# Kernel tuning notes

Measured on AMD Instinct MI355X. Metric: run time of the kernel, lower is better.

Reference implementation:

```python
import jax, jax.numpy as jnp
import numpy as np

B, L, D, DK, DV = 8, 2048, 1024, 1024, 1024

def setup_inputs() -> dict:
    key = jax.random.key(0)
    ks = jax.random.split(key, 8)
    # scale inputs/weights down so exp(scores) is numerically stable
    # (original softmax has no max-subtraction)
    x = jax.random.normal(ks[0], (B, L, D), dtype=jnp.float32) * 0.05
    Wq = jax.random.normal(ks[1], (D, DK), dtype=jnp.float32) * 0.05
    bq = jax.random.normal(ks[2], (DK,), dtype=jnp.float32) * 0.05
    Wk = jax.random.normal(ks[3], (D, DK), dtype=jnp.float32) * 0.05
    bk = jax.random.normal(ks[4], (DK,), dtype=jnp.float32) * 0.05
    Wv = jax.random.normal(ks[5], (D, DV), dtype=jnp.float32) * 0.05
    bv = jax.random.normal(ks[6], (DV,), dtype=jnp.float32) * 0.05
    actulength = jax.random.randint(ks[7], (B,), 1, L, dtype=jnp.int32)
    return {"x": x, "actulength": actulength, "Wq": Wq, "bq": bq,
            "Wk": Wk, "bk": bk, "Wv": Wv, "bv": bv}

def reference(x, actulength, Wq, bq, Wk, bk, Wv, bv):
    # QKV projections
    Q = x @ Wq + bq                      # [B, L, DK]
    K = x @ Wk + bk                      # [B, L, DK]
    V = x @ Wv + bv                      # [B, L, DV]
    scale = 1.0 / jnp.sqrt(jnp.float32(DK))
    scores = jnp.einsum('bld,bmd->blm', Q, K) * scale  # [B, L, L]
    # custom padding-aware softmax: subtract padding count from the sum
    s = jnp.exp(scores)
    tsum = jnp.sum(s, axis=2)            # [B, L]
    padding = (L - actulength).astype(s.dtype)[:, None]  # [B, 1]
    atten = s / (tsum - padding)[:, :, None]
    return jnp.einsum('blm,bmv->blv', atten, V)  # [B, L, DV]
```

## Files before the change

### kernel.cpp

```cpp
#include <hip/hip_runtime.h>
#include <hip/hip_bf16.h>
#include <cstdint>

#define DEV __device__ __forceinline__

typedef __attribute__((ext_vector_type(8))) __bf16 bf16x8;
typedef __attribute__((ext_vector_type(4))) float f32x4;

DEV ushort f2bf(float f){
  uint32_t u = __builtin_bit_cast(uint32_t, f);
  u += 0x7fffu + ((u >> 16) & 1u);
  return (ushort)(u >> 16);
}

DEV void gll16(const void* g, void* l){
  __builtin_amdgcn_global_load_lds((const __attribute__((address_space(1))) void*)g,
                                   (__attribute__((address_space(3))) void*)l, 16, 0, 0);
}

template<int MODE>
__global__ __launch_bounds__(512, 2) void gemm256(
    const ushort* __restrict__ A, const ushort* __restrict__ Bt,
    const float* __restrict__ bias,
    ushort* __restrict__ Cb, float* __restrict__ Cf,
    int gm, int gn, int K, int lda, int ldb, int ldc,
    size_t sA, size_t sB, size_t sC,
    float scale, float* __restrict__ partial, const float* __restrict__ denom,
    int Mrows, int nch)
{
  __shared__ __align__(16) ushort As[4][128][64];
  __shared__ __align__(16) ushort Bs[4][128][64];

  const int tid  = threadIdx.x;
  const int lane = tid & 63, wid = tid >> 6;
  const int wm = wid >> 2, wn = wid & 3;
  const int lr = lane & 15, fq = lane >> 4;
  const int lrh = lr >> 1;
  const int lo2 = ((lane & 1) << 2) | fq;

  const int nwg = gridDim.x;
  const int per = nwg >> 3;
  const int id  = blockIdx.x;
  const int swz = (id & 7) * per + (id >> 3);
  const int gmn = gm * gn;
  const int bz  = swz / gmn;
  const int rr  = swz - bz * gmn;
  const int bn  = rr / gm;
  const int bm  = rr - bn * gm;

  const ushort* Ab = A  + (size_t)bz * sA + (size_t)bm * 256 * (size_t)lda;
  const ushort* Bb = Bt + (size_t)bz * sB + (size_t)bn * 256 * (size_t)ldb;
  const int NT = K >> 5;

  auto stageA = [&](int t){
    const int s = t & 3;
    const size_t kb = (size_t)t * 64;
#pragma unroll
    for (int q = 0; q < 2; ++q){
      int c = q*512 + tid;
      int R = c >> 3, ci = c & 7;
      int u = ci ^ (R & 7);
      size_t sb = (size_t)(2*R + (u >> 2)) * (size_t)(lda*2) + kb + (size_t)((u & 3) << 4);
      gll16((const char*)Ab + sb,
            (ushort*)As + (size_t)s*8192 + (size_t)(q*512 + (wid << 6))*8);
    }
  };
  auto stageB = [&](int t){
    const int s = t & 3;
    const size_t kb = (size_t)t * 64;
#pragma unroll
    for (int q = 0; q < 2; ++q){
      int c = q*512 + tid;
      int R = c >> 3, ci = c & 7;
      int u = ci ^ (R & 7);
      size_t sb = (size_t)(2*R + (u >> 2)) * (size_t)(ldb*2) + kb + (size_t)((u & 3) << 4);
      gll16((const char*)Bb + sb,
            (ushort*)Bs + (size_t)s*8192 + (size_t)(q*512 + (wid << 6))*8);
    }
  };

  f32x4 acc[8][4];
  const f32x4 z = {0.f, 0.f, 0.f, 0.f};
#pragma unroll
  for (int m = 0; m < 8; ++m)
#pragma unroll
    for (int n = 0; n < 4; ++n) acc[m][n] = z;

  const int cio  = (lo2 ^ lrh) << 3;
  const int aoff = (wm*64 + lrh)*64 + cio;
  const int boff = (wn*32 + lrh)*64 + cio;

  stageA(0); stageB(0); stageA(1); stageB(1);
  asm volatile("s_waitcnt vmcnt(4)" ::: "memory");
  __builtin_amdgcn_s_barrier();

  for (int t = 0; t < NT; ++t){
    const int s = t & 3;
    const ushort* Asl = (const ushort*)As + (size_t)s*8192;
    const ushort* Bsl = (const ushort*)Bs + (size_t)s*8192;
    const bool pre = (t + 2 < NT);

    bf16x8 bfv[4], af0[4];
#pragma unroll
    for (int n = 0; n < 4; ++n)
      bfv[n] = *(const bf16x8*)&Bsl[boff + n*512];
#pragma unroll
    for (int m = 0; m < 4; ++m)
      af0[m] = *(const bf16x8*)&Asl[aoff + m*512];
    if (pre) stageA(t + 2);
    __builtin_amdgcn_s_barrier();
    asm volatile("s_waitcnt lgkmcnt(0)" ::: "memory");
    __builtin_amdgcn_sched_barrier(0);
    __builtin_amdgcn_s_setprio(1);
#pragma unroll
    for (int m = 0; m < 4; ++m)
#pragma unroll
      for (int n = 0; n < 4; ++n)
        acc[m][n] = __builtin_amdgcn_mfma_f32_16x16x32_bf16(af0[m], bfv[n], acc[m][n], 0, 0, 0);
    __builtin_amdgcn_s_setprio(0);
    __builtin_amdgcn_s_barrier();

    bf16x8 af1[4];
#pragma unroll
    for (int m = 0; m < 4; ++m)
      af1[m] = *(const bf16x8*)&Asl[aoff + (m + 4)*512];
    if (pre) stageB(t + 2);
    __builtin_amdgcn_s_barrier();
    asm volatile("s_waitcnt lgkmcnt(0)" ::: "memory");
    __builtin_amdgcn_sched_barrier(0);
    __builtin_amdgcn_s_setprio(1);
#pragma unroll
    for (int m = 0; m < 4; ++m)
#pragma unroll
      for (int n = 0; n < 4; ++n)
        acc[m + 4][n] = __builtin_amdgcn_mfma_f32_16x16x32_bf16(af1[m], bfv[n], acc[m + 4][n], 0, 0, 0);
    __builtin_amdgcn_s_setprio(0);

    if (t < NT - 1){
      if (t + 2 < NT) asm volatile("s_waitcnt vmcnt(4)" ::: "memory");
      else            asm volatile("s_waitcnt vmcnt(0)" ::: "memory");
      __builtin_amdgcn_s_barrier();
    }
  }

  const int rbase = bm*256 + wm*128 + fq*4;
  const int cbase = bn*256 + wn*64 + lr;

  if (MODE == 0){
    ushort* dst = Cb + (size_t)bz * sC;
#pragma unroll
    for (int m = 0; m < 8; ++m){
      int r0 = rbase + m*16;
#pragma unroll
      for (int n = 0; n < 4; ++n){
        int c = cbase + n*16;
        float bvv = bias[c];
#pragma unroll
        for (int i = 0; i < 4; ++i)
          dst[(size_t)(r0 + i)*ldc + c] = f2bf(acc[m][n][i] + bvv);
      }
    }
  } else if (MODE == 1){
    ushort* dst = Cb + (size_t)bz * sC;
#pragma unroll
    for (int m = 0; m < 8; ++m){
      int r0 = rbase + m*16;
#pragma unroll
      for (int i = 0; i < 4; ++i){
        int r = r0 + i;
        float rs = 0.f;
#pragma unroll
        for (int n = 0; n < 4; ++n){
          float v = __expf(acc[m][n][i] * scale);
          dst[(size_t)r*ldc + cbase + n*16] = f2bf(v);
          rs += v;
        }
        rs += __shfl_xor(rs, 1);
        rs += __shfl_xor(rs, 2);
        rs += __shfl_xor(rs, 4);
        rs += __shfl_xor(rs, 8);
        if (lr == 0)
          partial[((size_t)bz*Mrows + r)*nch + (bn*4 + wn)] = rs;
      }
    }
  } else {
    float* dst = Cf + (size_t)bz * sC;
#pragma unroll
    for (int m = 0; m < 8; ++m){
      int r0 = rbase + m*16;
#pragma unroll
      for (int i = 0; i < 4; ++i){
        int r = r0 + i;
        float inv = 1.0f / denom[(size_t)bz*Mrows + r];
#pragma unroll
        for (int n = 0; n < 4; ++n)
          dst[(size_t)r*ldc + cbase + n*16] = acc[m][n][i] * inv;
      }
    }
  }
}


__global__ void denom_k(const float* __restrict__ partial, const int* __restrict__ alen,
                        float* __restrict__ denom, int L, int nch){
  int i = blockIdx.x*blockDim.x + threadIdx.x;
  int b = i / L;
  const float* p = partial + (size_t)i*nch;
  float s = 0.f;
  for (int j = 0; j < nch; j++) s += p[j];
  denom[i] = s - (float)(L - alen[b]);
}

__global__ void cvt_f32_bf16(const float* __restrict__ in, ushort* __restrict__ out, long n4){
  long i = (long)blockIdx.x*blockDim.x + threadIdx.x;
  if (i >= n4) return;
  float4 f = ((const float4*)in)[i];
  ushort4 u;
  u.x = f2bf(f.x); u.y = f2bf(f.y); u.z = f2bf(f.z); u.w = f2bf(f.w);
  ((ushort4*)out)[i] = u;
}

__global__ __launch_bounds__(256) void transpose_f32_bf16(
    const float* __restrict__ in, ushort* __restrict__ out, int R, int C){
  __shared__ ushort t[32][33];
  int tx = threadIdx.x, ty = threadIdx.y;
  int c0 = blockIdx.x*32, r0 = blockIdx.y*32;
#pragma unroll
  for (int i = 0; i < 4; i++)
    t[ty + i*8][tx] = f2bf(in[(size_t)(r0 + ty + i*8)*C + c0 + tx]);
  __syncthreads();
#pragma unroll
  for (int i = 0; i < 4; i++)
    out[(size_t)(c0 + ty + i*8)*R + r0 + tx] = t[tx][ty + i*8];
}

__global__ __launch_bounds__(256) void transpose_v(
    const ushort* __restrict__ qkv, ushort* __restrict__ vt,
    int L_, int DV_, int ldq){
  __shared__ ushort tbuf[32][33];
  int bz = blockIdx.z;
  const ushort* src = qkv + (size_t)bz*L_*ldq + 2048;
  ushort* dst = vt + (size_t)bz*DV_*L_;
  int tx = threadIdx.x, ty = threadIdx.y;
  int c0 = blockIdx.x*32, r0 = blockIdx.y*32;
#pragma unroll
  for (int i = 0; i < 4; i++)
    tbuf[ty + i*8][tx] = src[(size_t)(r0 + ty + i*8)*ldq + c0 + tx];
  __syncthreads();
#pragma unroll
  for (int i = 0; i < 4; i++)
    dst[(size_t)(c0 + ty + i*8)*L_ + r0 + tx] = tbuf[tx][ty + i*8];
}

__global__ void pack_bias(const float* __restrict__ q, const float* __restrict__ k,
                          const float* __restrict__ v, float* __restrict__ o){
  int i = blockIdx.x*blockDim.x + threadIdx.x;
  o[i] = (i < 1024) ? q[i] : (i < 2048 ? k[i-1024] : v[i-2048]);
}


extern "C" void kernel_launch(void* const* d_in, const int* in_sizes, int n_in,
                              void* d_out, int out_size, void* d_ws, size_t ws_size,
                              hipStream_t stream){
  const int B = 8, L = 2048, D = 1024, DK = 1024, DV = 1024;
  const float scale = 0.03125f;

  const float* x  = (const float*)d_in[0];
  const int* alen = (const int*)d_in[1];
  const float* Wq = (const float*)d_in[2];
  const float* bq = (const float*)d_in[3];
  const float* Wk = (const float*)d_in[4];
  const float* bk = (const float*)d_in[5];
  const float* Wv = (const float*)d_in[6];
  const float* bv = (const float*)d_in[7];
  float* out = (float*)d_out;

  char* ws = (char*)d_ws;
  size_t off = 0;
  auto alloc = [&](size_t bytes) -> void* {
    void* p = ws + off;
    off += (bytes + 255) & ~(size_t)255;
    return p;
  };
  ushort* xb     = (ushort*)alloc((size_t)B*L*D*2);
  ushort* wqkvT  = (ushort*)alloc((size_t)3*DK*D*2);
  float*  bqkv   = (float*)alloc((size_t)3*DK*4);
  ushort* QKV    = (ushort*)alloc((size_t)B*L*3*DK*2);
  ushort* S      = (ushort*)alloc((size_t)B*L*L*2);
  float* partial = (float*)alloc((size_t)B*L*32*4);
  float* denom   = (float*)alloc((size_t)B*L*4);
  ushort* VTb    = xb;
  if (off > ws_size) return;

  dim3 tb(32, 8);

  long n4 = (long)B*L*D/4;
  cvt_f32_bf16<<<dim3((unsigned)((n4 + 255)/256)), 256, 0, stream>>>(x, xb, n4);

  transpose_f32_bf16<<<dim3(DK/32, D/32), tb, 0, stream>>>(Wq, wqkvT,             D, DK);
  transpose_f32_bf16<<<dim3(DK/32, D/32), tb, 0, stream>>>(Wk, wqkvT + DK*D,      D, DK);
  transpose_f32_bf16<<<dim3(DV/32, D/32), tb, 0, stream>>>(Wv, wqkvT + 2*DK*D,    D, DV);
  pack_bias<<<dim3(12), 256, 0, stream>>>(bq, bk, bv, bqkv);

  gemm256<0><<<dim3(64*12), 512, 0, stream>>>(
      xb, wqkvT, bqkv, QKV, nullptr, 64, 12, D, D, D, 3*DK,
      0, 0, 0, 0.f, nullptr, nullptr, 0, 0);

  transpose_v<<<dim3(DV/32, L/32, B), tb, 0, stream>>>(QKV, VTb, L, DV, 3*DK);

  gemm256<1><<<dim3(8*8*8), 512, 0, stream>>>(
      QKV , QKV + DK , nullptr, S, nullptr, 8, 8, DK, 3*DK, 3*DK, L,
      (size_t)L*3*DK, (size_t)L*3*DK, (size_t)L*L, scale, partial, nullptr, L, 32);

  denom_k<<<dim3(B*L/256), 256, 0, stream>>>(partial, alen, denom, L, 32);

  gemm256<2><<<dim3(8*4*8), 512, 0, stream>>>(
      S, VTb, nullptr, nullptr, out, 8, 4, L, L, L, DV,
      (size_t)L*L, (size_t)DV*L, (size_t)L*DV, 1.f, nullptr, denom, L, 0);
}
```

Before: 317.9 us.

## Fuse V transpose into QKV GEMM epilogue and deepen prefetch to three stages

The QKV projection GEMM now writes the V columns directly in transposed layout into a dedicated VT buffer, which removes the separate transpose_v kernel and its extra read and write of V. Q and K are stored in a narrower buffer with row stride 2*DK. The GEMM pipeline prefetches three stages ahead instead of two, with adjusted vmcnt waits, and the global-to-LDS address math is hoisted out of the staging lambdas. The transposed stores write 4 contiguous bf16 per lane along L, which may coalesce less well than row-major stores. The deeper prefetch keeps more loads in flight per wave.

```diff
diff --git a/kernel.cpp b/kernel.cpp
--- a/kernel.cpp
+++ b/kernel.cpp
@@ -22,7 +22,7 @@
 __global__ __launch_bounds__(512, 2) void gemm256(
     const ushort* __restrict__ A, const ushort* __restrict__ Bt,
     const float* __restrict__ bias,
-    ushort* __restrict__ Cb, float* __restrict__ Cf,
+    ushort* __restrict__ Cb, float* __restrict__ Cf, ushort* __restrict__ VTout,
     int gm, int gn, int K, int lda, int ldb, int ldc,
     size_t sA, size_t sB, size_t sC,
     float scale, float* __restrict__ partial, const float* __restrict__ denom,
@@ -52,31 +52,30 @@
   const ushort* Bb = Bt + (size_t)bz * sB + (size_t)bn * 256 * (size_t)ldb;
   const int NT = K >> 5;
 
+  auto srcOff = [&](int c, int ld)->size_t{
+    int R = c >> 3, ci = c & 7, u = ci ^ (R & 7);
+    return (size_t)(2*R + (u >> 2)) * (size_t)(ld*2) + (size_t)((u & 3) << 4);
+  };
+  const char* srcA0 = (const char*)Ab + srcOff(tid,       lda);
+  const char* srcA1 = (const char*)Ab + srcOff(512 + tid, lda);
+  const char* srcB0 = (const char*)Bb + srcOff(tid,       ldb);
+  const char* srcB1 = (const char*)Bb + srcOff(512 + tid, ldb);
+  char* AsB = (char*)As;
+  char* BsB = (char*)Bs;
+  const int dst0 = (wid << 6) * 16;
+  const int dst1 = (512 + (wid << 6)) * 16;
+
   auto stageA = [&](int t){
-    const int s = t & 3;
-    const size_t kb = (size_t)t * 64;
-#pragma unroll
-    for (int q = 0; q < 2; ++q){
-      int c = q*512 + tid;
-      int R = c >> 3, ci = c & 7;
-      int u = ci ^ (R & 7);
-      size_t sb = (size_t)(2*R + (u >> 2)) * (size_t)(lda*2) + kb + (size_t)((u & 3) << 4);
-      gll16((const char*)Ab + sb,
-            (ushort*)As + (size_t)s*8192 + (size_t)(q*512 + (wid << 6))*8);
-    }
+    const int sb = (t & 3) << 14;
+    const size_t kb = (size_t)t << 6;
+    gll16(srcA0 + kb, AsB + sb + dst0);
+    gll16(srcA1 + kb, AsB + sb + dst1);
   };
   auto stageB = [&](int t){
-    const int s = t & 3;
-    const size_t kb = (size_t)t * 64;
-#pragma unroll
-    for (int q = 0; q < 2; ++q){
-      int c = q*512 + tid;
-      int R = c >> 3, ci = c & 7;
-      int u = ci ^ (R & 7);
-      size_t sb = (size_t)(2*R + (u >> 2)) * (size_t)(ldb*2) + kb + (size_t)((u & 3) << 4);
-      gll16((const char*)Bb + sb,
-            (ushort*)Bs + (size_t)s*8192 + (size_t)(q*512 + (wid << 6))*8);
-    }
+    const int sb = (t & 3) << 14;
+    const size_t kb = (size_t)t << 6;
+    gll16(srcB0 + kb, BsB + sb + dst0);
+    gll16(srcB1 + kb, BsB + sb + dst1);
   };
 
   f32x4 acc[8][4];
@@ -90,15 +89,15 @@
   const int aoff = (wm*64 + lrh)*64 + cio;
   const int boff = (wn*32 + lrh)*64 + cio;
 
-  stageA(0); stageB(0); stageA(1); stageB(1);
-  asm volatile("s_waitcnt vmcnt(4)" ::: "memory");
+  stageA(0); stageB(0); stageA(1); stageB(1); stageA(2); stageB(2);
+  asm volatile("s_waitcnt vmcnt(8)" ::: "memory");
   __builtin_amdgcn_s_barrier();
 
   for (int t = 0; t < NT; ++t){
     const int s = t & 3;
     const ushort* Asl = (const ushort*)As + (size_t)s*8192;
     const ushort* Bsl = (const ushort*)Bs + (size_t)s*8192;
-    const bool pre = (t + 2 < NT);
+    const bool pre = (t + 3 < NT);
 
     bf16x8 bfv[4], af0[4];
 #pragma unroll
@@ -107,7 +106,7 @@
 #pragma unroll
     for (int m = 0; m < 4; ++m)
       af0[m] = *(const bf16x8*)&Asl[aoff + m*512];
-    if (pre) stageA(t + 2);
+    if (pre) stageA(t + 3);
     __builtin_amdgcn_s_barrier();
     asm volatile("s_waitcnt lgkmcnt(0)" ::: "memory");
     __builtin_amdgcn_sched_barrier(0);
@@ -124,7 +123,7 @@
 #pragma unroll
     for (int m = 0; m < 4; ++m)
       af1[m] = *(const bf16x8*)&Asl[aoff + (m + 4)*512];
-    if (pre) stageB(t + 2);
+    if (pre) stageB(t + 3);
     __builtin_amdgcn_s_barrier();
     asm volatile("s_waitcnt lgkmcnt(0)" ::: "memory");
     __builtin_amdgcn_sched_barrier(0);
@@ -137,8 +136,9 @@
     __builtin_amdgcn_s_setprio(0);
 
     if (t < NT - 1){
-      if (t + 2 < NT) asm volatile("s_waitcnt vmcnt(4)" ::: "memory");
-      else            asm volatile("s_waitcnt vmcnt(0)" ::: "memory");
+      if      (t + 3 < NT) asm volatile("s_waitcnt vmcnt(8)" ::: "memory");
+      else if (t + 2 < NT) asm volatile("s_waitcnt vmcnt(4)" ::: "memory");
+      else                 asm volatile("s_waitcnt vmcnt(0)" ::: "memory");
       __builtin_amdgcn_s_barrier();
     }
   }
@@ -147,17 +147,37 @@
   const int cbase = bn*256 + wn*64 + lr;
 
   if (MODE == 0){
-    ushort* dst = Cb + (size_t)bz * sC;
-#pragma unroll
-    for (int m = 0; m < 8; ++m){
-      int r0 = rbase + m*16;
-#pragma unroll
-      for (int n = 0; n < 4; ++n){
-        int c = cbase + n*16;
-        float bvv = bias[c];
-#pragma unroll
-        for (int i = 0; i < 4; ++i)
-          dst[(size_t)(r0 + i)*ldc + c] = f2bf(acc[m][n][i] + bvv);
+    if (bn >= 8){
+#pragma unroll
+      for (int m = 0; m < 8; ++m){
+        int r0 = rbase + m*16;
+        int b = r0 >> 11, l = r0 & 2047;
+        ushort* vb = VTout + (size_t)b * 1024 * 2048;
+#pragma unroll
+        for (int n = 0; n < 4; ++n){
+          int c = cbase + n*16;
+          float bvv = bias[c];
+          ushort4 u4;
+          u4.x = f2bf(acc[m][n][0] + bvv);
+          u4.y = f2bf(acc[m][n][1] + bvv);
+          u4.z = f2bf(acc[m][n][2] + bvv);
+          u4.w = f2bf(acc[m][n][3] + bvv);
+          *(ushort4*)&vb[(size_t)(c - 2048)*2048 + l] = u4;
+        }
+      }
+    } else {
+      ushort* dst = Cb + (size_t)bz * sC;
+#pragma unroll
+      for (int m = 0; m < 8; ++m){
+        int r0 = rbase + m*16;
+#pragma unroll
+        for (int n = 0; n < 4; ++n){
+          int c = cbase + n*16;
+          float bvv = bias[c];
+#pragma unroll
+          for (int i = 0; i < 4; ++i)
+            dst[(size_t)(r0 + i)*ldc + c] = f2bf(acc[m][n][i] + bvv);
+        }
       }
     }
   } else if (MODE == 1){
@@ -234,24 +254,6 @@
     out[(size_t)(c0 + ty + i*8)*R + r0 + tx] = t[tx][ty + i*8];
 }
 
-__global__ __launch_bounds__(256) void transpose_v(
-    const ushort* __restrict__ qkv, ushort* __restrict__ vt,
-    int L_, int DV_, int ldq){
-  __shared__ ushort tbuf[32][33];
-  int bz = blockIdx.z;
-  const ushort* src = qkv + (size_t)bz*L_*ldq + 2048;
-  ushort* dst = vt + (size_t)bz*DV_*L_;
-  int tx = threadIdx.x, ty = threadIdx.y;
-  int c0 = blockIdx.x*32, r0 = blockIdx.y*32;
-#pragma unroll
-  for (int i = 0; i < 4; i++)
-    tbuf[ty + i*8][tx] = src[(size_t)(r0 + ty + i*8)*ldq + c0 + tx];
-  __syncthreads();
-#pragma unroll
-  for (int i = 0; i < 4; i++)
-    dst[(size_t)(c0 + ty + i*8)*L_ + r0 + tx] = tbuf[tx][ty + i*8];
-}
-
 __global__ void pack_bias(const float* __restrict__ q, const float* __restrict__ k,
                           const float* __restrict__ v, float* __restrict__ o){
   int i = blockIdx.x*blockDim.x + threadIdx.x;
@@ -285,11 +287,11 @@
   ushort* xb     = (ushort*)alloc((size_t)B*L*D*2);
   ushort* wqkvT  = (ushort*)alloc((size_t)3*DK*D*2);
   float*  bqkv   = (float*)alloc((size_t)3*DK*4);
-  ushort* QKV    = (ushort*)alloc((size_t)B*L*3*DK*2);
+  ushort* QK     = (ushort*)alloc((size_t)B*L*2*DK*2);
+  ushort* VTb    = (ushort*)alloc((size_t)B*DV*L*2);
   ushort* S      = (ushort*)alloc((size_t)B*L*L*2);
   float* partial = (float*)alloc((size_t)B*L*32*4);
   float* denom   = (float*)alloc((size_t)B*L*4);
-  ushort* VTb    = xb;
   if (off > ws_size) return;
 
   dim3 tb(32, 8);
@@ -297,24 +299,23 @@
   long n4 = (long)B*L*D/4;
   cvt_f32_bf16<<<dim3((unsigned)((n4 + 255)/256)), 256, 0, stream>>>(x, xb, n4);
 
-  transpose_f32_bf16<<<dim3(DK/32, D/32), tb, 0, stream>>>(Wq, wqkvT,             D, DK);
-  transpose_f32_bf16<<<dim3(DK/32, D/32), tb, 0, stream>>>(Wk, wqkvT + DK*D,      D, DK);
-  transpose_f32_bf16<<<dim3(DV/32, D/32), tb, 0, stream>>>(Wv, wqkvT + 2*DK*D,    D, DV);
+  transpose_f32_bf16<<<dim3(DK/32, D/32), tb, 0, stream>>>(Wq, wqkvT,          D, DK);
+  transpose_f32_bf16<<<dim3(DK/32, D/32), tb, 0, stream>>>(Wk, wqkvT + DK*D,   D, DK);
+  transpose_f32_bf16<<<dim3(DV/32, D/32), tb, 0, stream>>>(Wv, wqkvT + 2*DK*D, D, DV);
   pack_bias<<<dim3(12), 256, 0, stream>>>(bq, bk, bv, bqkv);
 
   gemm256<0><<<dim3(64*12), 512, 0, stream>>>(
-      xb, wqkvT, bqkv, QKV, nullptr, 64, 12, D, D, D, 3*DK,
+      xb, wqkvT, bqkv, QK, nullptr, VTb, 64, 12, D, D, D, 2*DK,
       0, 0, 0, 0.f, nullptr, nullptr, 0, 0);
 
-  transpose_v<<<dim3(DV/32, L/32, B), tb, 0, stream>>>(QKV, VTb, L, DV, 3*DK);
-
   gemm256<1><<<dim3(8*8*8), 512, 0, stream>>>(
-      QKV , QKV + DK , nullptr, S, nullptr, 8, 8, DK, 3*DK, 3*DK, L,
-      (size_t)L*3*DK, (size_t)L*3*DK, (size_t)L*L, scale, partial, nullptr, L, 32);
+      QK , QK + DK , nullptr, S, nullptr, nullptr, 8, 8, DK,
+      2*DK, 2*DK, L,
+      (size_t)L*2*DK, (size_t)L*2*DK, (size_t)L*L, scale, partial, nullptr, L, 32);
 
   denom_k<<<dim3(B*L/256), 256, 0, stream>>>(partial, alen, denom, L, 32);
 
   gemm256<2><<<dim3(8*4*8), 512, 0, stream>>>(
-      S, VTb, nullptr, nullptr, out, 8, 4, L, L, L, DV,
+      S, VTb, nullptr, nullptr, out, nullptr, 8, 4, L, L, L, DV,
       (size_t)L*L, (size_t)DV*L, (size_t)L*DV, 1.f, nullptr, denom, L, 0);
 }
```

After: 311.3 us. -2.1%, faster.
